# Optimization experiments

Measured on AMD Instinct MI355X. Metric: run time of the kernel, lower is better.

## Reference

```python
import jax, jax.numpy as jnp
import numpy as np

N = 1 << 20        # number of query points
L_HIDDEN = 6       # hidden (64->64) layers, i.e. params[1:-1]
NEG_SLOPE = 0.2    # nn.LeakyReLU(0.2)

# NOTE: nn.Dropout(0.5) is treated in eval mode (identity), the standard
# convention for deterministic correctness baselines.

def _lrelu(x):
    return jnp.where(x >= 0, x, NEG_SLOPE * x)


def setup_inputs() -> dict:
    key = jax.random.key(0)
    ks = jax.random.split(key, 11)
    return {
        "points": jax.random.normal(ks[0], (N, 3), jnp.float32),
        "w0": jax.random.normal(ks[1], (3, 64), jnp.float32),
        "s0": jax.random.normal(ks[2], (64,), jnp.float32),
        "b0": jax.random.normal(ks[3], (64,), jnp.float32),
        "wh": jax.random.normal(ks[4], (L_HIDDEN, 64, 64), jnp.float32),
        "sh": jax.random.normal(ks[5], (L_HIDDEN, 64), jnp.float32),
        "bh": jax.random.normal(ks[6], (L_HIDDEN, 64), jnp.float32),
        "wo": jax.random.normal(ks[7], (64, 1), jnp.float32),
        "so": jax.random.normal(ks[8], (), jnp.float32),
        "bo": jax.random.normal(ks[9], (), jnp.float32),
    }


def reference(points, w0, s0, b0, wh, sh, bh, wo, so, bo):
    # first layer: [N,3] @ [3,64] * scale + bias -> leakyrelu
    x = _lrelu(jnp.matmul(points, w0) * s0 + b0)
    # hidden layers: small static loop over structurally distinct param sets
    for i in range(L_HIDDEN):
        x = _lrelu(jnp.matmul(x, wh[i]) * sh[i] + bh[i])
    # output layer: [N,64] @ [64,1] * scalar + scalar (no activation)
    return jnp.matmul(x, wo) * so + bo
```

## Files before the change

kernel.cpp:

```cpp
#include <hip/hip_runtime.h>


typedef _Float16 half8 __attribute__((ext_vector_type(8)));
typedef _Float16 half2v __attribute__((ext_vector_type(2)));
typedef float floatx16 __attribute__((ext_vector_type(16)));
typedef float float2v __attribute__((ext_vector_type(2)));

#define N_HID 6
#define OFF_A 0
#define LDS_BYTES 49152
#define OFF_B 49152
#define OFF_D 51200
#define OFF_E 51456
#define SETUP_TOTAL (24576 + 1024 + 64 + 1024)

__global__ __launch_bounds__(256) void setup_weights(
    const float* __restrict__ w0, const float* __restrict__ s0, const float* __restrict__ b0,
    const float* __restrict__ wh, const float* __restrict__ sh, const float* __restrict__ bh,
    const float* __restrict__ wo, const float* __restrict__ so,
    unsigned char* __restrict__ ws)
{
    int i = blockIdx.x * 256 + threadIdx.x;
    if (i < 24576) {
        int j = i & 7, lane = (i >> 3) & 63, s = (i >> 9) & 3, t = (i >> 11) & 1, l = i >> 12;
        int m = 32 * t + (lane & 31);
        int h = lane >> 5;
        int feat = 16 * s + 8 * (j >> 2) + 4 * h + (j & 3);
        ((_Float16*)(ws + OFF_A))[i] = (_Float16)(wh[(l * 64 + feat) * 64 + m] * sh[l * 64 + m]);
    } else if (i < 24576 + 1024) {
        int i2 = i - 24576;
        int j = i2 & 7, lane = (i2 >> 3) & 63, t = i2 >> 9;
        int m = 32 * t + (lane & 31);
        int k = 8 * (lane >> 5) + j;
        float v = (k < 3) ? w0[k * 64 + m] * s0[m] * 0.015625f
                          : (k == 3 ? b0[m] * 0.015625f : 0.f);
        ((_Float16*)(ws + OFF_B))[i2] = (_Float16)v;
    } else if (i < 24576 + 1024 + 64) {
        int i2 = i - 24576 - 1024;
        int r = i2 & 15, t = (i2 >> 4) & 1, h = i2 >> 5;
        int feat = 32 * t + (r & 3) + 8 * ((r >> 2) & 3) + 4 * h;
        ((float*)(ws + OFF_D))[i2] = wo[feat] * so[0] * 64.f;
    } else if (i < SETUP_TOTAL) {
        int i2 = i - 24576 - 1024 - 64;
        int j = i2 & 7, lane = (i2 >> 3) & 63, t = i2 >> 9;
        int m = 32 * t + (lane & 31);
        int h = lane >> 5;
        float v = (h == 0 && j < N_HID) ? bh[j * 64 + m] * 0.015625f : 0.f;
        ((_Float16*)(ws + OFF_E))[i2] = (_Float16)v;
    }
}

union FragU { int i[4]; half8 v; };

static __device__ __forceinline__ int pkrtz(float a, float b) {
    auto hh = __builtin_amdgcn_cvt_pkrtz(a, b);
    int r;
    __builtin_memcpy(&r, &hh, 4);
    return r;
}

static __device__ __forceinline__ int lrelu2(int v) {
    half2v u;
    __builtin_memcpy(&u, &v, 4);
    half2v w = u * (_Float16)0.2f;
    half2v r = __builtin_elementwise_max(u, w);
    int o;
    __builtin_memcpy(&o, &r, 4);
    return o;
}

static __device__ __forceinline__ floatx16 mfma16(half8 a, half8 b, floatx16 c) {
    return __builtin_amdgcn_mfma_f32_32x32x16_f16(a, b, c, 0, 0, 0);
}

__global__ __launch_bounds__(256, 3) void mlp_mfma(
    const float* __restrict__ points,
    const unsigned char* __restrict__ ws,
    const float* __restrict__ bo,
    float* __restrict__ out, int n)
{
    __shared__ __align__(16) unsigned char lds[LDS_BYTES];

    const int lane = threadIdx.x & 63;
    const int wv = threadIdx.x >> 6;
    const int p = lane & 31;
    const int h = lane >> 5;
    const int base = (blockIdx.x * 4 + wv) * 64;
    const int pt0 = base + p, pt1 = base + 32 + p;
    const int pl0 = min(pt0, n - 1), pl1 = min(pt1, n - 1);

    const float P0x = points[3 * pl0], P0y = points[3 * pl0 + 1], P0z = points[3 * pl0 + 2];
    const float P1x = points[3 * pl1], P1y = points[3 * pl1 + 1], P1z = points[3 * pl1 + 2];
    const half8* Eg = (const half8*)(ws + OFF_E);
    const half8 biasAll0 = Eg[lane];
    const half8 biasAll1 = Eg[64 + lane];
    const half8* A0g = (const half8*)(ws + OFF_B);
    const half8 W0a = A0g[lane];
    const half8 W0b = A0g[64 + lane];
    const float bov = bo[0];

    {
        const uint4* src = (const uint4*)ws;
        uint4* dst = (uint4*)lds;
#pragma unroll
        for (int i = 0; i < 12; ++i) {
            int idx = threadIdx.x + 256 * i;
            dst[idx] = src[idx];
        }
    }
    __syncthreads();

    const half8* Wf = (const half8*)(lds + OFF_A);

    floatx16 acc0[2], acc1[2];

    {
        FragU bu0, bu1;
        bu0.i[0] = bu0.i[1] = bu0.i[2] = bu0.i[3] = 0;
        bu1 = bu0;
        if (h == 0) {
            bu0.v[0] = (_Float16)P0x; bu0.v[1] = (_Float16)P0y;
            bu0.v[2] = (_Float16)P0z; bu0.v[3] = (_Float16)1.0f;
            bu1.v[0] = (_Float16)P1x; bu1.v[1] = (_Float16)P1y;
            bu1.v[2] = (_Float16)P1z; bu1.v[3] = (_Float16)1.0f;
        }
        const floatx16 z = (floatx16)(0.0f);
        acc0[0] = mfma16(W0a, bu0.v, z);
        acc0[1] = mfma16(W0b, bu0.v, z);
        acc1[0] = mfma16(W0a, bu1.v, z);
        acc1[1] = mfma16(W0b, bu1.v, z);
    }

#pragma unroll
    for (int l = 0; l < N_HID; ++l) {
        FragU f0[4], f1[4];
#pragma unroll
        for (int s = 0; s < 4; ++s) {
            const int t = s >> 1, rpb = 4 * (s & 1);
#pragma unroll
            for (int c = 0; c < 4; ++c) {
                f0[s].i[c] = lrelu2(pkrtz(acc0[t][2 * (rpb + c)], acc0[t][2 * (rpb + c) + 1]));
                f1[s].i[c] = lrelu2(pkrtz(acc1[t][2 * (rpb + c)], acc1[t][2 * (rpb + c) + 1]));
            }
        }
        FragU e;
        e.i[0] = e.i[1] = e.i[2] = e.i[3] = 0;
        if (h == 0) e.i[l >> 1] = (l & 1) ? 0x3C000000 : 0x00003C00;
        const half8* wl = Wf + l * 512 + lane;
        const floatx16 z = (floatx16)(0.0f);

        floatx16 bc0 = mfma16(biasAll0, e.v, z);
        floatx16 n00, n10;
#pragma unroll
        for (int s = 0; s < 4; ++s) {
            half8 wt = wl[s * 64];
            n00 = mfma16(wt, f0[s].v, (s == 0) ? bc0 : n00);
            n10 = mfma16(wt, f1[s].v, (s == 0) ? bc0 : n10);
        }
        floatx16 bc1 = mfma16(biasAll1, e.v, z);
        floatx16 n01, n11;
#pragma unroll
        for (int s = 0; s < 4; ++s) {
            half8 wt = wl[256 + s * 64];
            n01 = mfma16(wt, f0[s].v, (s == 0) ? bc1 : n01);
            n11 = mfma16(wt, f1[s].v, (s == 0) ? bc1 : n11);
        }
        acc0[0] = n00; acc0[1] = n01; acc1[0] = n10; acc1[1] = n11;
    }

    {
        const floatx16* woG = (const floatx16*)(ws + OFF_D);
        floatx16 wo0 = woG[h * 2 + 0];
        floatx16 wo1 = woG[h * 2 + 1];
        float2v q0 = {0.f, 0.f}, q1 = {0.f, 0.f};
#pragma unroll
        for (int r2 = 0; r2 < 8; ++r2) {
            float2v w0p = { wo0[2 * r2], wo0[2 * r2 + 1] };
            float2v w1p = { wo1[2 * r2], wo1[2 * r2 + 1] };
            float2v u;
            u.x = acc0[0][2 * r2]; u.y = acc0[0][2 * r2 + 1];
            u = __builtin_elementwise_max(u, 0.2f * u);
            q0 += u * w0p;
            u.x = acc0[1][2 * r2]; u.y = acc0[1][2 * r2 + 1];
            u = __builtin_elementwise_max(u, 0.2f * u);
            q0 += u * w1p;
            u.x = acc1[0][2 * r2]; u.y = acc1[0][2 * r2 + 1];
            u = __builtin_elementwise_max(u, 0.2f * u);
            q1 += u * w0p;
            u.x = acc1[1][2 * r2]; u.y = acc1[1][2 * r2 + 1];
            u = __builtin_elementwise_max(u, 0.2f * u);
            q1 += u * w1p;
        }
        float part0 = q0.x + q0.y;
        float part1 = q1.x + q1.y;
        part0 += __shfl_xor(part0, 32);
        part1 += __shfl_xor(part1, 32);
        if (h == 0) {
            if (pt0 < n) out[pt0] = part0 + bov;
            if (pt1 < n) out[pt1] = part1 + bov;
        }
    }
}

extern "C" void kernel_launch(void* const* d_in, const int* in_sizes, int n_in,
                              void* d_out, int out_size, void* d_ws, size_t ws_size,
                              hipStream_t stream) {
    const float* points = (const float*)d_in[0];
    const float* w0     = (const float*)d_in[1];
    const float* s0     = (const float*)d_in[2];
    const float* b0     = (const float*)d_in[3];
    const float* wh     = (const float*)d_in[4];
    const float* sh     = (const float*)d_in[5];
    const float* bh     = (const float*)d_in[6];
    const float* wo     = (const float*)d_in[7];
    const float* so     = (const float*)d_in[8];
    const float* bo     = (const float*)d_in[9];

    const int n = in_sizes[0] / 3;

    setup_weights<<<(SETUP_TOTAL + 255) / 256, 256, 0, stream>>>(
        w0, s0, b0, wh, sh, bh, wo, so, (unsigned char*)d_ws);

    const int grid = (n + 255) / 256;
    mlp_mfma<<<grid, 256, 0, stream>>>(
        points, (const unsigned char*)d_ws, bo, (float*)d_out, n);
}
```

Before: 134.0 us.

## Use persistent grid-stride waves with prefetch of next point batch

Launches a fixed grid of 512 blocks whose waves loop over 64-point batches in grid-stride order. The 48KB weight copy into LDS then happens once per block rather than once per 256 points, and each iteration prefetches the next batch's points while the current batch's MFMAs run. The trade-offs are a few more live registers and a fixed grid that may not fill every CU evenly with 3 blocks per CU.

```diff
diff --git a/kernel.cpp b/kernel.cpp
--- a/kernel.cpp
+++ b/kernel.cpp
@@ -7,6 +7,8 @@
 typedef float float2v __attribute__((ext_vector_type(2)));
 
 #define N_HID 6
+#define NBLOCKS 512
+#define NWAVES (NBLOCKS * 4)
 #define OFF_A 0
 #define LDS_BYTES 49152
 #define OFF_B 49152
@@ -85,12 +87,7 @@
     const int wv = threadIdx.x >> 6;
     const int p = lane & 31;
     const int h = lane >> 5;
-    const int base = (blockIdx.x * 4 + wv) * 64;
-    const int pt0 = base + p, pt1 = base + 32 + p;
-    const int pl0 = min(pt0, n - 1), pl1 = min(pt1, n - 1);
-
-    const float P0x = points[3 * pl0], P0y = points[3 * pl0 + 1], P0z = points[3 * pl0 + 2];
-    const float P1x = points[3 * pl1], P1y = points[3 * pl1 + 1], P1z = points[3 * pl1 + 2];
+
     const half8* Eg = (const half8*)(ws + OFF_E);
     const half8 biasAll0 = Eg[lane];
     const half8 biasAll1 = Eg[64 + lane];
@@ -111,94 +108,124 @@
     __syncthreads();
 
     const half8* Wf = (const half8*)(lds + OFF_A);
-
-    floatx16 acc0[2], acc1[2];
-
+    const floatx16* woG = (const floatx16*)(ws + OFF_D);
+
+    const int nbatch = (n + 63) >> 6;
+    const int gw = blockIdx.x * 4 + wv;
+    int b = gw;
+    if (b >= nbatch) return;
+
+    float P0x, P0y, P0z, P1x, P1y, P1z;
     {
-        FragU bu0, bu1;
-        bu0.i[0] = bu0.i[1] = bu0.i[2] = bu0.i[3] = 0;
-        bu1 = bu0;
-        if (h == 0) {
-            bu0.v[0] = (_Float16)P0x; bu0.v[1] = (_Float16)P0y;
-            bu0.v[2] = (_Float16)P0z; bu0.v[3] = (_Float16)1.0f;
-            bu1.v[0] = (_Float16)P1x; bu1.v[1] = (_Float16)P1y;
-            bu1.v[2] = (_Float16)P1z; bu1.v[3] = (_Float16)1.0f;
-        }
-        const floatx16 z = (floatx16)(0.0f);
-        acc0[0] = mfma16(W0a, bu0.v, z);
-        acc0[1] = mfma16(W0b, bu0.v, z);
-        acc1[0] = mfma16(W0a, bu1.v, z);
-        acc1[1] = mfma16(W0b, bu1.v, z);
-    }
-
-#pragma unroll
-    for (int l = 0; l < N_HID; ++l) {
-        FragU f0[4], f1[4];
-#pragma unroll
-        for (int s = 0; s < 4; ++s) {
-            const int t = s >> 1, rpb = 4 * (s & 1);
-#pragma unroll
-            for (int c = 0; c < 4; ++c) {
-                f0[s].i[c] = lrelu2(pkrtz(acc0[t][2 * (rpb + c)], acc0[t][2 * (rpb + c) + 1]));
-                f1[s].i[c] = lrelu2(pkrtz(acc1[t][2 * (rpb + c)], acc1[t][2 * (rpb + c) + 1]));
-            }
-        }
-        FragU e;
-        e.i[0] = e.i[1] = e.i[2] = e.i[3] = 0;
-        if (h == 0) e.i[l >> 1] = (l & 1) ? 0x3C000000 : 0x00003C00;
-        const half8* wl = Wf + l * 512 + lane;
-        const floatx16 z = (floatx16)(0.0f);
-
-        floatx16 bc0 = mfma16(biasAll0, e.v, z);
-        floatx16 n00, n10;
-#pragma unroll
-        for (int s = 0; s < 4; ++s) {
-            half8 wt = wl[s * 64];
-            n00 = mfma16(wt, f0[s].v, (s == 0) ? bc0 : n00);
-            n10 = mfma16(wt, f1[s].v, (s == 0) ? bc0 : n10);
-        }
-        floatx16 bc1 = mfma16(biasAll1, e.v, z);
-        floatx16 n01, n11;
-#pragma unroll
-        for (int s = 0; s < 4; ++s) {
-            half8 wt = wl[256 + s * 64];
-            n01 = mfma16(wt, f0[s].v, (s == 0) ? bc1 : n01);
-            n11 = mfma16(wt, f1[s].v, (s == 0) ? bc1 : n11);
-        }
-        acc0[0] = n00; acc0[1] = n01; acc1[0] = n10; acc1[1] = n11;
-    }
-
-    {
-        const floatx16* woG = (const floatx16*)(ws + OFF_D);
-        floatx16 wo0 = woG[h * 2 + 0];
-        floatx16 wo1 = woG[h * 2 + 1];
-        float2v q0 = {0.f, 0.f}, q1 = {0.f, 0.f};
-#pragma unroll
-        for (int r2 = 0; r2 < 8; ++r2) {
-            float2v w0p = { wo0[2 * r2], wo0[2 * r2 + 1] };
-            float2v w1p = { wo1[2 * r2], wo1[2 * r2 + 1] };
-            float2v u;
-            u.x = acc0[0][2 * r2]; u.y = acc0[0][2 * r2 + 1];
-            u = __builtin_elementwise_max(u, 0.2f * u);
-            q0 += u * w0p;
-            u.x = acc0[1][2 * r2]; u.y = acc0[1][2 * r2 + 1];
-            u = __builtin_elementwise_max(u, 0.2f * u);
-            q0 += u * w1p;
-            u.x = acc1[0][2 * r2]; u.y = acc1[0][2 * r2 + 1];
-            u = __builtin_elementwise_max(u, 0.2f * u);
-            q1 += u * w0p;
-            u.x = acc1[1][2 * r2]; u.y = acc1[1][2 * r2 + 1];
-            u = __builtin_elementwise_max(u, 0.2f * u);
-            q1 += u * w1p;
-        }
-        float part0 = q0.x + q0.y;
-        float part1 = q1.x + q1.y;
-        part0 += __shfl_xor(part0, 32);
-        part1 += __shfl_xor(part1, 32);
-        if (h == 0) {
-            if (pt0 < n) out[pt0] = part0 + bov;
-            if (pt1 < n) out[pt1] = part1 + bov;
-        }
+        int q0 = min(b * 64 + p, n - 1), q1 = min(b * 64 + 32 + p, n - 1);
+        P0x = points[3 * q0]; P0y = points[3 * q0 + 1]; P0z = points[3 * q0 + 2];
+        P1x = points[3 * q1]; P1y = points[3 * q1 + 1]; P1z = points[3 * q1 + 2];
+    }
+
+    while (true) {
+        const int nb = b + NWAVES;
+        const bool more = nb < nbatch;
+        float N0x, N0y, N0z, N1x, N1y, N1z;
+        N0x = N0y = N0z = N1x = N1y = N1z = 0.f;
+        if (more) {
+            int q0 = min(nb * 64 + p, n - 1), q1 = min(nb * 64 + 32 + p, n - 1);
+            N0x = points[3 * q0]; N0y = points[3 * q0 + 1]; N0z = points[3 * q0 + 2];
+            N1x = points[3 * q1]; N1y = points[3 * q1 + 1]; N1z = points[3 * q1 + 2];
+        }
+
+        floatx16 acc0[2], acc1[2];
+
+        {
+            FragU bu0, bu1;
+            bu0.i[0] = bu0.i[1] = bu0.i[2] = bu0.i[3] = 0;
+            bu1 = bu0;
+            if (h == 0) {
+                bu0.v[0] = (_Float16)P0x; bu0.v[1] = (_Float16)P0y;
+                bu0.v[2] = (_Float16)P0z; bu0.v[3] = (_Float16)1.0f;
+                bu1.v[0] = (_Float16)P1x; bu1.v[1] = (_Float16)P1y;
+                bu1.v[2] = (_Float16)P1z; bu1.v[3] = (_Float16)1.0f;
+            }
+            const floatx16 z = (floatx16)(0.0f);
+            acc0[0] = mfma16(W0a, bu0.v, z);
+            acc0[1] = mfma16(W0b, bu0.v, z);
+            acc1[0] = mfma16(W0a, bu1.v, z);
+            acc1[1] = mfma16(W0b, bu1.v, z);
+        }
+
+#pragma unroll
+        for (int l = 0; l < N_HID; ++l) {
+            FragU f0[4], f1[4];
+#pragma unroll
+            for (int s = 0; s < 4; ++s) {
+                const int t = s >> 1, rpb = 4 * (s & 1);
+#pragma unroll
+                for (int c = 0; c < 4; ++c) {
+                    f0[s].i[c] = lrelu2(pkrtz(acc0[t][2 * (rpb + c)], acc0[t][2 * (rpb + c) + 1]));
+                    f1[s].i[c] = lrelu2(pkrtz(acc1[t][2 * (rpb + c)], acc1[t][2 * (rpb + c) + 1]));
+                }
+            }
+            FragU e;
+            e.i[0] = e.i[1] = e.i[2] = e.i[3] = 0;
+            if (h == 0) e.i[l >> 1] = (l & 1) ? 0x3C000000 : 0x00003C00;
+            const half8* wl = Wf + l * 512 + lane;
+            const floatx16 z = (floatx16)(0.0f);
+
+            floatx16 bc0 = mfma16(biasAll0, e.v, z);
+            floatx16 n00, n10;
+#pragma unroll
+            for (int s = 0; s < 4; ++s) {
+                half8 wt = wl[s * 64];
+                n00 = mfma16(wt, f0[s].v, (s == 0) ? bc0 : n00);
+                n10 = mfma16(wt, f1[s].v, (s == 0) ? bc0 : n10);
+            }
+            floatx16 bc1 = mfma16(biasAll1, e.v, z);
+            floatx16 n01, n11;
+#pragma unroll
+            for (int s = 0; s < 4; ++s) {
+                half8 wt = wl[256 + s * 64];
+                n01 = mfma16(wt, f0[s].v, (s == 0) ? bc1 : n01);
+                n11 = mfma16(wt, f1[s].v, (s == 0) ? bc1 : n11);
+            }
+            acc0[0] = n00; acc0[1] = n01; acc1[0] = n10; acc1[1] = n11;
+        }
+
+        {
+            floatx16 wo0 = woG[h * 2 + 0];
+            floatx16 wo1 = woG[h * 2 + 1];
+            float2v q0 = {0.f, 0.f}, q1 = {0.f, 0.f};
+#pragma unroll
+            for (int r2 = 0; r2 < 8; ++r2) {
+                float2v w0p = { wo0[2 * r2], wo0[2 * r2 + 1] };
+                float2v w1p = { wo1[2 * r2], wo1[2 * r2 + 1] };
+                float2v u;
+                u.x = acc0[0][2 * r2]; u.y = acc0[0][2 * r2 + 1];
+                u = __builtin_elementwise_max(u, 0.2f * u);
+                q0 += u * w0p;
+                u.x = acc0[1][2 * r2]; u.y = acc0[1][2 * r2 + 1];
+                u = __builtin_elementwise_max(u, 0.2f * u);
+                q0 += u * w1p;
+                u.x = acc1[0][2 * r2]; u.y = acc1[0][2 * r2 + 1];
+                u = __builtin_elementwise_max(u, 0.2f * u);
+                q1 += u * w0p;
+                u.x = acc1[1][2 * r2]; u.y = acc1[1][2 * r2 + 1];
+                u = __builtin_elementwise_max(u, 0.2f * u);
+                q1 += u * w1p;
+            }
+            float part0 = q0.x + q0.y;
+            float part1 = q1.x + q1.y;
+            part0 += __shfl_xor(part0, 32);
+            part1 += __shfl_xor(part1, 32);
+            if (h == 0) {
+                int pt0 = b * 64 + p, pt1 = b * 64 + 32 + p;
+                if (pt0 < n) out[pt0] = part0 + bov;
+                if (pt1 < n) out[pt1] = part1 + bov;
+            }
+        }
+
+        if (!more) break;
+        P0x = N0x; P0y = N0y; P0z = N0z;
+        P1x = N1x; P1y = N1y; P1z = N1z;
+        b = nb;
     }
 }
 
@@ -221,7 +248,6 @@
     setup_weights<<<(SETUP_TOTAL + 255) / 256, 256, 0, stream>>>(
         w0, s0, b0, wh, sh, bh, wo, so, (unsigned char*)d_ws);
 
-    const int grid = (n + 255) / 256;
-    mlp_mfma<<<grid, 256, 0, stream>>>(
+    mlp_mfma<<<NBLOCKS, 256, 0, stream>>>(
         points, (const unsigned char*)d_ws, bo, (float*)d_out, n);
 }
```

Result: slower. 237.6 us (+77.4%).
